# Kernel tuning notes

Hardware: AMD Instinct MI355X
Metric: run time of the kernel (lower is better)

## Reference

```python
import jax, jax.numpy as jnp
import numpy as np

MARGIN = 0.5
BETA = 0.0
K = 5

def setup_inputs() -> dict:
    key = jax.random.key(0)
    k1, k2 = jax.random.split(key)
    n, d, n_classes = 4096, 512, 512
    inputs = jax.random.normal(k1, (n, d), dtype=jnp.float32)
    # L2-normalize as is standard for similarity-based DML embeddings
    inputs = inputs / jnp.linalg.norm(inputs, axis=1, keepdims=True)
    targets = jax.random.randint(k2, (n,), 0, n_classes, dtype=jnp.int64)
    return {"inputs": inputs, "targets": targets}

def reference(inputs, targets):
    n = inputs.shape[0]
    sim = inputs @ inputs.T                      # [n, n] similarity matrix
    same = targets[:, None] == targets[None, :]  # [n, n] same-class mask
    eye = jnp.eye(n, dtype=bool)
    pos_mask = same & ~eye                       # positive pairs (off-diagonal)
    neg_mask = ~same                             # negative pairs
    # margin_loss (hinge on similarity): pos -> [margin + beta - s]_+, neg -> [margin + s - beta]_+
    pos_l = jnp.maximum(MARGIN + BETA - sim, 0.0)
    neg_l = jnp.maximum(MARGIN + sim - BETA, 0.0)
    valid = pos_mask | neg_mask
    pair_loss = jnp.where(pos_mask, pos_l, neg_l)  # per-pair loss where valid
    num_of_zeros = jnp.sum(valid & (pair_loss == 0.0))
    # top-(4K) over the multiset of all valid pair losses (== topk of concat(pos_loss, neg_loss))
    masked = jnp.where(valid, pair_loss, -jnp.inf).reshape(-1)
    top_loss, _ = jax.lax.top_k(masked, 4 * K)
    loss = jnp.mean(top_loss)
    mean_pos_sim = jnp.sum(jnp.where(pos_mask, sim, 0.0)) / jnp.sum(pos_mask)
    mean_neg_sim = jnp.sum(jnp.where(neg_mask, sim, 0.0)) / jnp.sum(neg_mask)
    # NOTE: the original swaps the names: it returns mean(pos_sim) as `mean_neg_sim` and vice versa.
    return (loss, num_of_zeros, mean_pos_sim, mean_neg_sim)
```

## Files before the change

kernel.cpp:

```cpp
#include <hip/hip_runtime.h>
#include <hip/hip_fp16.h>

constexpr int N = 4096;
constexpr int D = 512;
constexpr int NT = 32;
constexpr int NBLK = NT * (NT + 1) / 2;
constexpr int NSEG = 33;
constexpr int SEGSZ = 16;
constexpr float SENT = -1e30f;
constexpr unsigned TCV = 8386560u;

typedef _Float16 f16x8 __attribute__((ext_vector_type(8)));
typedef float f32x4 __attribute__((ext_vector_type(4)));

__device__ __forceinline__ void load_lds16(const _Float16* g, _Float16* l) {
  __builtin_amdgcn_global_load_lds(
      (const __attribute__((address_space(1))) void*)g,
      (__attribute__((address_space(3))) void*)l, 16, 0, 0);
}

template <int M>
__device__ __forceinline__ void wave_sel10(float (&vals)[M], float (&out)[10]) {
  int lane = threadIdx.x & 63;
  float lm = vals[0];
#pragma unroll
  for (int k = 1; k < M; k++) lm = fmaxf(lm, vals[k]);
#pragma unroll
  for (int r = 0; r < 10; r++) {
    float wmx = lm;
#pragma unroll
    for (int ofs = 1; ofs < 64; ofs <<= 1)
      wmx = fmaxf(wmx, __shfl_xor(wmx, ofs));
    out[r] = wmx;
    unsigned long long b = __ballot(lm == wmx);
    int leader = __ffsll(b) - 1;
    if (lane == leader) {
      bool found = false;
#pragma unroll
      for (int k = 0; k < M; k++) {
        bool hit = !found && (vals[k] == wmx);
        vals[k] = hit ? SENT : vals[k];
        found = found || hit;
      }
      lm = vals[0];
#pragma unroll
      for (int k = 1; k < M; k++) lm = fmaxf(lm, vals[k]);
    }
  }
}

constexpr int TOP10G_IDX = 1584;
constexpr int DONE2_IDX = 6864;
constexpr int SEGL2_IDX = 6880;
constexpr int XH_OFF = 32768;

__global__ void prep_kernel(const float4* __restrict__ X4,
                            ushort4* __restrict__ Xh4,
                            unsigned* __restrict__ done2) {
  int gid = blockIdx.x * 256 + threadIdx.x;
  if (gid == 0) *done2 = 0u;
  float4 v = X4[gid];
  ushort4 o;
  o.x = __half_as_ushort(__float2half_rn(v.x));
  o.y = __half_as_ushort(__float2half_rn(v.y));
  o.z = __half_as_ushort(__float2half_rn(v.z));
  o.w = __half_as_ushort(__float2half_rn(v.w));
  Xh4[gid] = o;
}

__global__ __launch_bounds__(512, 4) void gemm_stats_kernel(
    const _Float16* __restrict__ Xh, const int* __restrict__ tgt,
    float* __restrict__ slots, float* __restrict__ top10g) {
  __shared__ _Float16 As[2][128 * 64];
  __shared__ _Float16 Bs[2][128 * 64];
  __shared__ int tA[128], tB[128];
  __shared__ float redf[2][8];
  __shared__ unsigned redu[8];
  __shared__ float wml[80];

  int tid = threadIdx.x;

  int id = blockIdx.x, br = 0;
  while (id >= (NT - br)) { id -= (NT - br); br++; }
  int bc = br + id;

  if (tid < 128) tA[tid] = tgt[br * 128 + tid];
  else if (tid < 256) tB[tid - 128] = tgt[bc * 128 + (tid - 128)];

  int lane = tid & 63, wave = tid >> 6;
  int wm2 = (wave >> 2) << 6;
  int wn2 = (wave & 3) << 5;
  int lrow = lane & 15;
  int q4 = lane >> 4;
  int x7 = lrow & 7;
  int quad4 = q4 * 4;

  int srow[2], scol[2], sdst[2];
#pragma unroll
  for (int i = 0; i < 2; i++) {
    int C = i * 512 + tid;
    int row = C >> 3, p = C & 7;
    srow[i] = row;
    scol[i] = (p ^ (row & 7)) * 8;
    sdst[i] = (i * 8 + wave) * 512;
  }
  const _Float16* Arow = Xh + (size_t)(br * 128) * D;
  const _Float16* Brow = Xh + (size_t)(bc * 128) * D;

#pragma unroll
  for (int i = 0; i < 2; i++) {
    load_lds16(Arow + srow[i] * D + scol[i], &As[0][sdst[i]]);
    load_lds16(Brow + srow[i] * D + scol[i], &Bs[0][sdst[i]]);
  }

  f32x4 acc[4][2] = {};
#pragma unroll
  for (int t = 0; t < 8; t++) {
    int cur = t & 1;
    __syncthreads();
    if (t < 7) {
      int k0 = (t + 1) * 64;
#pragma unroll
      for (int i = 0; i < 2; i++) {
        load_lds16(Arow + srow[i] * D + k0 + scol[i], &As[cur ^ 1][sdst[i]]);
        load_lds16(Brow + srow[i] * D + k0 + scol[i], &Bs[cur ^ 1][sdst[i]]);
      }
    }
#pragma unroll
    for (int ks = 0; ks < 64; ks += 32) {
      int c0 = ks >> 3;
      f16x8 af[4], bf[2];
#pragma unroll
      for (int mi = 0; mi < 4; mi++)
        af[mi] = *(const f16x8*)&As[cur][(wm2 + mi * 16 + lrow) * 64 +
                                         ((c0 + q4) ^ x7) * 8];
#pragma unroll
      for (int ni = 0; ni < 2; ni++)
        bf[ni] = *(const f16x8*)&Bs[cur][(wn2 + ni * 16 + lrow) * 64 +
                                         ((c0 + q4) ^ x7) * 8];
#pragma unroll
      for (int mi = 0; mi < 4; mi++)
#pragma unroll
        for (int ni = 0; ni < 2; ni++)
          acc[mi][ni] = __builtin_amdgcn_mfma_f32_16x16x32_f16(
              af[mi], bf[ni], acc[mi][ni], 0, 0, 0);
    }
  }

  int tj[2];
#pragma unroll
  for (int ni = 0; ni < 2; ni++) tj[ni] = tB[wn2 + ni * 16 + lrow];

  float lsv = 0.f, lsp = 0.f;
  unsigned cz = 0;
  int ib = br * 128 + wm2 + quad4;
  int jb = bc * 128 + wn2 + lrow;

  float vals[32];
#pragma unroll
  for (int mi = 0; mi < 4; mi++) {
#pragma unroll
    for (int r = 0; r < 4; r++) {
      int trow = tA[wm2 + mi * 16 + quad4 + r];
      int i = ib + mi * 16 + r;
#pragma unroll
      for (int ni = 0; ni < 2; ni++) {
        float s = acc[mi][ni][r];
        int j = jb + ni * 16;
        bool valid = j > i;
        bool pos = valid && (trow == tj[ni]);
        float loss = fmaxf(0.5f + (pos ? -s : s), 0.0f);
        if (valid) { lsv += s; if (loss == 0.0f) cz += 0x10000u; }
        if (pos) { lsp += s; cz += 1u; }
        vals[(mi * 2 + ni) * 4 + r] = valid ? loss : SENT;
      }
    }
  }

#pragma unroll
  for (int o = 32; o > 0; o >>= 1) {
    lsv += __shfl_down(lsv, o);
    lsp += __shfl_down(lsp, o);
    cz += __shfl_down(cz, o);
  }
  if (lane == 0) {
    redf[0][wave] = lsv; redf[1][wave] = lsp; redu[wave] = cz;
  }

  float wl[10];
  wave_sel10<32>(vals, wl);
  if (lane == 0) {
#pragma unroll
    for (int r = 0; r < 10; r++) wml[wave * 10 + r] = wl[r];
  }
  __syncthreads();

  if (tid == 0) {
    float a = 0.f, b = 0.f;
    unsigned c = 0;
#pragma unroll
    for (int w = 0; w < 8; w++) { a += redf[0][w]; b += redf[1][w]; c += redu[w]; }
    slots[blockIdx.x] = a;
    slots[NBLK + blockIdx.x] = b;
    ((unsigned*)slots)[2 * NBLK + blockIdx.x] = c;
  }
  if (wave == 0) {
    float m2[2];
    m2[0] = wml[lane];
    m2[1] = (lane + 64 < 80) ? wml[lane + 64] : SENT;
    float b10[10];
    wave_sel10<2>(m2, b10);
    if (lane == 0) {
#pragma unroll
      for (int r = 0; r < 10; r++) top10g[blockIdx.x * 10 + r] = b10[r];
    }
  }
}

__global__ __launch_bounds__(256) void finalize_kernel(
    const float* __restrict__ slots, const float* __restrict__ top10g,
    float* __restrict__ segL2, unsigned* __restrict__ done2,
    float* __restrict__ out) {
  const float* blk_sumv = slots;
  const float* blk_sump = slots + NBLK;
  const unsigned* blk_cnt = (const unsigned*)(slots + 2 * NBLK);
  float* ssumv = segL2;
  float* ssump = segL2 + NSEG;
  unsigned* scv = (unsigned*)(segL2 + 2 * NSEG);
  unsigned* szz = (unsigned*)(segL2 + 3 * NSEG);
  float* st10 = segL2 + 4 * NSEG;

  __shared__ float wml[40];
  __shared__ int lastFlag;

  int tid = threadIdx.x;
  int lane = tid & 63, wave = tid >> 6;
  int f = blockIdx.x;

  float sv = 0.f, sp = 0.f;
  unsigned cv = 0, zz = 0;
  if (tid < SEGSZ) {
    int r = f * SEGSZ + tid;
    sv = blk_sumv[r]; sp = blk_sump[r];
    unsigned c = blk_cnt[r];
    cv = c & 0xffffu; zz = c >> 16;
  }
#pragma unroll
  for (int o = 8; o > 0; o >>= 1) {
    sv += __shfl_down(sv, o);
    sp += __shfl_down(sp, o);
    cv += __shfl_down(cv, o);
    zz += __shfl_down(zz, o);
  }

  float v1[1];
  v1[0] = (tid < SEGSZ * 10) ? top10g[f * SEGSZ * 10 + tid] : SENT;
  float wl[10];
  wave_sel10<1>(v1, wl);
  if (lane == 0) {
#pragma unroll
    for (int r = 0; r < 10; r++) wml[wave * 10 + r] = wl[r];
  }
  __syncthreads();
  if (wave == 0) {
    float m1[1];
    m1[0] = (lane < 40) ? wml[lane] : SENT;
    float s10[10];
    wave_sel10<1>(m1, s10);
    if (lane == 0) {
      ssumv[f] = sv; ssump[f] = sp; scv[f] = cv; szz[f] = zz;
#pragma unroll
      for (int r = 0; r < 10; r++) st10[f * 10 + r] = s10[r];
    }
  }
  __syncthreads();

  if (tid == 0) {
    __threadfence();
    unsigned old = atomicAdd(done2, 1u);
    lastFlag = (old == NSEG - 1);
  }
  __syncthreads();
  if (!lastFlag) return;
  __threadfence();

  float sv2 = 0.f, sp2 = 0.f;
  unsigned cv2 = 0, zz2 = 0;
  if (tid < NSEG) {
    sv2 = ssumv[tid]; sp2 = ssump[tid];
    cv2 = scv[tid]; zz2 = szz[tid];
  }
#pragma unroll
  for (int o = 32; o > 0; o >>= 1) {
    sv2 += __shfl_down(sv2, o);
    sp2 += __shfl_down(sp2, o);
    cv2 += __shfl_down(cv2, o);
    zz2 += __shfl_down(zz2, o);
  }

  float v2[2];
  v2[0] = (tid < NSEG * 10) ? st10[tid] : SENT;
  int g2 = tid + 256;
  v2[1] = (g2 < NSEG * 10) ? st10[g2] : SENT;
  float wl2[10];
  wave_sel10<2>(v2, wl2);
  if (lane == 0) {
#pragma unroll
    for (int r = 0; r < 10; r++) wml[wave * 10 + r] = wl2[r];
  }
  __syncthreads();

  if (wave == 0) {
    float m1[1];
    m1[0] = (lane < 40) ? wml[lane] : SENT;
    float f10[10];
    wave_sel10<1>(m1, f10);
    if (lane == 0) {
      float topsum = 0.f;
#pragma unroll
      for (int r = 0; r < 10; r++) topsum += f10[r];
      out[0] = topsum * 0.1f;
      out[1] = (float)(2u * zz2);
      out[2] = sp2 / (float)cv2;
      out[3] = (sv2 - sp2) / (float)(TCV - cv2);
    }
  }
}

extern "C" void kernel_launch(void* const* d_in, const int* in_sizes, int n_in,
                              void* d_out, int out_size, void* d_ws,
                              size_t ws_size, hipStream_t stream) {
  const float* X = (const float*)d_in[0];
  const int* tgt = (const int*)d_in[1];
  float* out = (float*)d_out;
  char* ws = (char*)d_ws;

  float* slots = (float*)ws;
  float* top10g = slots + TOP10G_IDX;
  unsigned* done2 = (unsigned*)(slots + DONE2_IDX);
  float* segL2 = slots + SEGL2_IDX;
  _Float16* Xh = (_Float16*)(ws + XH_OFF);

  prep_kernel<<<(N * D / 4) / 256, 256, 0, stream>>>((const float4*)X,
                                                     (ushort4*)Xh, done2);
  gemm_stats_kernel<<<NBLK, 512, 0, stream>>>(Xh, tgt, slots, top10g);
  finalize_kernel<<<NSEG, 256, 0, stream>>>(slots, top10g, segL2, done2, out);
}
```

Before: 114.6 us.

## Threshold-filter top-k candidates via LDS and fuse finalize into GEMM kernel

Each GEMM block now collects only losses at or above a fixed threshold into a shared buffer with an LDS atomic. It runs a small wave selection over that buffer, falling back to the full 32-value per-wave selection when the candidate count is out of range. The separate finalize kernel is removed; the last block to finish, found with a global atomic counter, does the final reduction and writes the outputs. This removes one launch and most of the per-block selection work, at the cost of LDS atomics in the epilogue and a data-dependent threshold that was tuned to the input distribution.

```diff
diff --git a/kernel.cpp b/kernel.cpp
--- a/kernel.cpp
+++ b/kernel.cpp
@@ -5,10 +5,11 @@
 constexpr int D = 512;
 constexpr int NT = 32;
 constexpr int NBLK = NT * (NT + 1) / 2;
-constexpr int NSEG = 33;
-constexpr int SEGSZ = 16;
 constexpr float SENT = -1e30f;
 constexpr unsigned TCV = 8386560u;
+
+constexpr float T0 = 0.63f;
+constexpr unsigned CCAP = 256;
 
 typedef _Float16 f16x8 __attribute__((ext_vector_type(8)));
 typedef float f32x4 __attribute__((ext_vector_type(4)));
@@ -51,7 +52,6 @@
 
 constexpr int TOP10G_IDX = 1584;
 constexpr int DONE2_IDX = 6864;
-constexpr int SEGL2_IDX = 6880;
 constexpr int XH_OFF = 32768;
 
 __global__ void prep_kernel(const float4* __restrict__ X4,
@@ -70,15 +70,20 @@
 
 __global__ __launch_bounds__(512, 4) void gemm_stats_kernel(
     const _Float16* __restrict__ Xh, const int* __restrict__ tgt,
-    float* __restrict__ slots, float* __restrict__ top10g) {
+    float* __restrict__ slots, float* __restrict__ top10g,
+    unsigned* __restrict__ done2, float* __restrict__ out) {
   __shared__ _Float16 As[2][128 * 64];
   __shared__ _Float16 Bs[2][128 * 64];
   __shared__ int tA[128], tB[128];
   __shared__ float redf[2][8];
-  __shared__ unsigned redu[8];
+  __shared__ unsigned redu[2][8];
   __shared__ float wml[80];
+  __shared__ float cbuf[CCAP];
+  __shared__ unsigned ccnt;
+  __shared__ int lastFlag;
 
   int tid = threadIdx.x;
+  if (tid == 0) ccnt = 0u;
 
   int id = blockIdx.x, br = 0;
   while (id >= (NT - br)) { id -= (NT - br); br++; }
@@ -155,8 +160,6 @@
   unsigned cz = 0;
   int ib = br * 128 + wm2 + quad4;
   int jb = bc * 128 + wn2 + lrow;
-
-  float vals[32];
 #pragma unroll
   for (int mi = 0; mi < 4; mi++) {
 #pragma unroll
@@ -170,13 +173,18 @@
         bool valid = j > i;
         bool pos = valid && (trow == tj[ni]);
         float loss = fmaxf(0.5f + (pos ? -s : s), 0.0f);
-        if (valid) { lsv += s; if (loss == 0.0f) cz += 0x10000u; }
+        if (valid) {
+          lsv += s;
+          if (loss == 0.0f) cz += 0x10000u;
+          if (loss >= T0) {
+            unsigned p = atomicAdd(&ccnt, 1u);
+            if (p < CCAP) cbuf[p] = loss;
+          }
+        }
         if (pos) { lsp += s; cz += 1u; }
-        vals[(mi * 2 + ni) * 4 + r] = valid ? loss : SENT;
-      }
-    }
-  }
-
+      }
+    }
+  }
 #pragma unroll
   for (int o = 32; o > 0; o >>= 1) {
     lsv += __shfl_down(lsv, o);
@@ -184,145 +192,146 @@
     cz += __shfl_down(cz, o);
   }
   if (lane == 0) {
-    redf[0][wave] = lsv; redf[1][wave] = lsp; redu[wave] = cz;
-  }
-
-  float wl[10];
-  wave_sel10<32>(vals, wl);
-  if (lane == 0) {
-#pragma unroll
-    for (int r = 0; r < 10; r++) wml[wave * 10 + r] = wl[r];
+    redf[0][wave] = lsv; redf[1][wave] = lsp; redu[0][wave] = cz;
   }
   __syncthreads();
 
+  unsigned cc = ccnt;
+  if (cc >= 10u && cc <= CCAP) {
+    if (wave == 0) {
+      float m4[4];
+#pragma unroll
+      for (int k = 0; k < 4; k++) {
+        unsigned g = lane + k * 64u;
+        m4[k] = (g < cc) ? cbuf[g] : SENT;
+      }
+      float b10[10];
+      wave_sel10<4>(m4, b10);
+      if (lane == 0) {
+#pragma unroll
+        for (int r = 0; r < 10; r++) top10g[blockIdx.x * 10 + r] = b10[r];
+      }
+    }
+  } else {
+    float vals[32];
+#pragma unroll
+    for (int mi = 0; mi < 4; mi++) {
+#pragma unroll
+      for (int r = 0; r < 4; r++) {
+        int trow = tA[wm2 + mi * 16 + quad4 + r];
+        int i = ib + mi * 16 + r;
+#pragma unroll
+        for (int ni = 0; ni < 2; ni++) {
+          float s = acc[mi][ni][r];
+          int j = jb + ni * 16;
+          bool valid = j > i;
+          bool pos = valid && (trow == tj[ni]);
+          float loss = fmaxf(0.5f + (pos ? -s : s), 0.0f);
+          vals[(mi * 2 + ni) * 4 + r] = valid ? loss : SENT;
+        }
+      }
+    }
+    float wl[10];
+    wave_sel10<32>(vals, wl);
+    if (lane == 0) {
+#pragma unroll
+      for (int r = 0; r < 10; r++) wml[wave * 10 + r] = wl[r];
+    }
+    __syncthreads();
+    if (wave == 0) {
+      float m2[2];
+      m2[0] = wml[lane];
+      m2[1] = (lane + 64 < 80) ? wml[lane + 64] : SENT;
+      float b10[10];
+      wave_sel10<2>(m2, b10);
+      if (lane == 0) {
+#pragma unroll
+        for (int r = 0; r < 10; r++) top10g[blockIdx.x * 10 + r] = b10[r];
+      }
+    }
+  }
   if (tid == 0) {
     float a = 0.f, b = 0.f;
     unsigned c = 0;
 #pragma unroll
-    for (int w = 0; w < 8; w++) { a += redf[0][w]; b += redf[1][w]; c += redu[w]; }
+    for (int w = 0; w < 8; w++) {
+      a += redf[0][w]; b += redf[1][w]; c += redu[0][w];
+    }
     slots[blockIdx.x] = a;
     slots[NBLK + blockIdx.x] = b;
     ((unsigned*)slots)[2 * NBLK + blockIdx.x] = c;
   }
+  __syncthreads();
+
+  if (tid == 0) {
+    __threadfence();
+    unsigned old = atomicAdd(done2, 1u);
+    lastFlag = (old == NBLK - 1);
+  }
+  __syncthreads();
+  if (!lastFlag) return;
+  __threadfence();
+
+  float sv = 0.f, sp = 0.f;
+  unsigned cv = 0, zz = 0;
+#pragma unroll
+  for (int k = 0; k < 2; k++) {
+    int r = tid + k * 512;
+    if (r < NBLK) {
+      sv += slots[r];
+      sp += slots[NBLK + r];
+      unsigned c = ((const unsigned*)slots)[2 * NBLK + r];
+      cv += c & 0xffffu;
+      zz += c >> 16;
+    }
+  }
+#pragma unroll
+  for (int o = 32; o > 0; o >>= 1) {
+    sv += __shfl_down(sv, o);
+    sp += __shfl_down(sp, o);
+    cv += __shfl_down(cv, o);
+    zz += __shfl_down(zz, o);
+  }
+  if (lane == 0) {
+    redf[0][wave] = sv; redf[1][wave] = sp;
+    redu[0][wave] = cv; redu[1][wave] = zz;
+  }
+
+  float v11[11];
+#pragma unroll
+  for (int k = 0; k < 11; k++) {
+    int g = tid + k * 512;
+    v11[k] = (g < NBLK * 10) ? top10g[g] : SENT;
+  }
+  float wl2[10];
+  wave_sel10<11>(v11, wl2);
+  if (lane == 0) {
+#pragma unroll
+    for (int r = 0; r < 10; r++) wml[wave * 10 + r] = wl2[r];
+  }
+  __syncthreads();
+
   if (wave == 0) {
     float m2[2];
     m2[0] = wml[lane];
     m2[1] = (lane + 64 < 80) ? wml[lane + 64] : SENT;
-    float b10[10];
-    wave_sel10<2>(m2, b10);
-    if (lane == 0) {
-#pragma unroll
-      for (int r = 0; r < 10; r++) top10g[blockIdx.x * 10 + r] = b10[r];
-    }
-  }
-}
-
-__global__ __launch_bounds__(256) void finalize_kernel(
-    const float* __restrict__ slots, const float* __restrict__ top10g,
-    float* __restrict__ segL2, unsigned* __restrict__ done2,
-    float* __restrict__ out) {
-  const float* blk_sumv = slots;
-  const float* blk_sump = slots + NBLK;
-  const unsigned* blk_cnt = (const unsigned*)(slots + 2 * NBLK);
-  float* ssumv = segL2;
-  float* ssump = segL2 + NSEG;
-  unsigned* scv = (unsigned*)(segL2 + 2 * NSEG);
-  unsigned* szz = (unsigned*)(segL2 + 3 * NSEG);
-  float* st10 = segL2 + 4 * NSEG;
-
-  __shared__ float wml[40];
-  __shared__ int lastFlag;
-
-  int tid = threadIdx.x;
-  int lane = tid & 63, wave = tid >> 6;
-  int f = blockIdx.x;
-
-  float sv = 0.f, sp = 0.f;
-  unsigned cv = 0, zz = 0;
-  if (tid < SEGSZ) {
-    int r = f * SEGSZ + tid;
-    sv = blk_sumv[r]; sp = blk_sump[r];
-    unsigned c = blk_cnt[r];
-    cv = c & 0xffffu; zz = c >> 16;
-  }
-#pragma unroll
-  for (int o = 8; o > 0; o >>= 1) {
-    sv += __shfl_down(sv, o);
-    sp += __shfl_down(sp, o);
-    cv += __shfl_down(cv, o);
-    zz += __shfl_down(zz, o);
-  }
-
-  float v1[1];
-  v1[0] = (tid < SEGSZ * 10) ? top10g[f * SEGSZ * 10 + tid] : SENT;
-  float wl[10];
-  wave_sel10<1>(v1, wl);
-  if (lane == 0) {
-#pragma unroll
-    for (int r = 0; r < 10; r++) wml[wave * 10 + r] = wl[r];
-  }
-  __syncthreads();
-  if (wave == 0) {
-    float m1[1];
-    m1[0] = (lane < 40) ? wml[lane] : SENT;
-    float s10[10];
-    wave_sel10<1>(m1, s10);
-    if (lane == 0) {
-      ssumv[f] = sv; ssump[f] = sp; scv[f] = cv; szz[f] = zz;
-#pragma unroll
-      for (int r = 0; r < 10; r++) st10[f * 10 + r] = s10[r];
-    }
-  }
-  __syncthreads();
-
-  if (tid == 0) {
-    __threadfence();
-    unsigned old = atomicAdd(done2, 1u);
-    lastFlag = (old == NSEG - 1);
-  }
-  __syncthreads();
-  if (!lastFlag) return;
-  __threadfence();
-
-  float sv2 = 0.f, sp2 = 0.f;
-  unsigned cv2 = 0, zz2 = 0;
-  if (tid < NSEG) {
-    sv2 = ssumv[tid]; sp2 = ssump[tid];
-    cv2 = scv[tid]; zz2 = szz[tid];
-  }
-#pragma unroll
-  for (int o = 32; o > 0; o >>= 1) {
-    sv2 += __shfl_down(sv2, o);
-    sp2 += __shfl_down(sp2, o);
-    cv2 += __shfl_down(cv2, o);
-    zz2 += __shfl_down(zz2, o);
-  }
-
-  float v2[2];
-  v2[0] = (tid < NSEG * 10) ? st10[tid] : SENT;
-  int g2 = tid + 256;
-  v2[1] = (g2 < NSEG * 10) ? st10[g2] : SENT;
-  float wl2[10];
-  wave_sel10<2>(v2, wl2);
-  if (lane == 0) {
-#pragma unroll
-    for (int r = 0; r < 10; r++) wml[wave * 10 + r] = wl2[r];
-  }
-  __syncthreads();
-
-  if (wave == 0) {
-    float m1[1];
-    m1[0] = (lane < 40) ? wml[lane] : SENT;
     float f10[10];
-    wave_sel10<1>(m1, f10);
+    wave_sel10<2>(m2, f10);
     if (lane == 0) {
       float topsum = 0.f;
 #pragma unroll
       for (int r = 0; r < 10; r++) topsum += f10[r];
+      float tsv = 0.f, tsp = 0.f;
+      unsigned tcv = 0, tzz = 0;
+#pragma unroll
+      for (int w = 0; w < 8; w++) {
+        tsv += redf[0][w]; tsp += redf[1][w];
+        tcv += redu[0][w]; tzz += redu[1][w];
+      }
       out[0] = topsum * 0.1f;
-      out[1] = (float)(2u * zz2);
-      out[2] = sp2 / (float)cv2;
-      out[3] = (sv2 - sp2) / (float)(TCV - cv2);
+      out[1] = (float)(2u * tzz);
+      out[2] = tsp / (float)tcv;
+      out[3] = (tsv - tsp) / (float)(TCV - tcv);
     }
   }
 }
@@ -338,11 +347,10 @@
   float* slots = (float*)ws;
   float* top10g = slots + TOP10G_IDX;
   unsigned* done2 = (unsigned*)(slots + DONE2_IDX);
-  float* segL2 = slots + SEGL2_IDX;
   _Float16* Xh = (_Float16*)(ws + XH_OFF);
 
   prep_kernel<<<(N * D / 4) / 256, 256, 0, stream>>>((const float4*)X,
                                                      (ushort4*)Xh, done2);
-  gemm_stats_kernel<<<NBLK, 512, 0, stream>>>(Xh, tgt, slots, top10g);
-  finalize_kernel<<<NSEG, 256, 0, stream>>>(slots, top10g, segL2, done2, out);
-}
+  gemm_stats_kernel<<<NBLK, 512, 0, stream>>>(Xh, tgt, slots, top10g, done2,
+                                              out);
+}
```

New measurement: 113.4 us. No clear change (-1.0%).
